# Kernel tuning notes

Hardware: AMD Instinct MI355X
Metric: run time of the kernel (lower is better)

## Reference

```python
import jax, jax.numpy as jnp
import numpy as np

L, B, T, C, H, V, CTX = 4, 2, 1024, 1024, 16, 50257, 2048
D = C // H
EPS = 1e-5
NEG_SLOPE = 0.01


def layer_norm(x, w, b):
    mu = jnp.mean(x, axis=-1, keepdims=True)
    var = jnp.mean(jnp.square(x - mu), axis=-1, keepdims=True)
    return (x - mu) * jax.lax.rsqrt(var + EPS) * w + b


def setup_inputs() -> dict:
    key = jax.random.key(0)
    ks = jax.random.split(key, 8)
    s = 0.02  # init std as in _init_weights
    return {
        "idx": jax.random.randint(ks[0], (B, T), 0, V),
        "wte": jax.random.normal(ks[1], (V, C), jnp.float32) * s,
        "wpe": jax.random.normal(ks[2], (CTX, C), jnp.float32) * s,
        "ln1_w": jnp.ones((L, C), jnp.float32),
        "ln1_b": jnp.zeros((L, C), jnp.float32),
        "attn_w": jax.random.normal(ks[3], (L, C, 3 * C), jnp.float32) * s,
        "attn_b": jnp.zeros((L, 3 * C), jnp.float32),
        "proj_w": jax.random.normal(ks[4], (L, C, C), jnp.float32) * s,
        "proj_b": jnp.zeros((L, C), jnp.float32),
        "ln2_w": jnp.ones((L, C), jnp.float32),
        "ln2_b": jnp.zeros((L, C), jnp.float32),
        "fc_w": jax.random.normal(ks[5], (L, C, 4 * C), jnp.float32) * s,
        "fc_b": jnp.zeros((L, 4 * C), jnp.float32),
        "fcproj_w": jax.random.normal(ks[6], (L, 4 * C, C), jnp.float32) * s,
        "fcproj_b": jnp.zeros((L, C), jnp.float32),
        "lnf_w": jnp.ones((C,), jnp.float32),
        "lnf_b": jnp.zeros((C,), jnp.float32),
    }


def reference(idx, wte, wpe, ln1_w, ln1_b, attn_w, attn_b, proj_w, proj_b,
              ln2_w, ln2_b, fc_w, fc_b, fcproj_w, fcproj_b, lnf_w, lnf_b):
    t = idx.shape[1]
    x = wte[idx] + wpe[:t]  # [B,T,C]; dropout=0 => identity
    causal = jnp.tril(jnp.ones((t, t), bool))  # [T,T]
    scale = 1.0 / np.sqrt(D)
    for l in range(L):
        # --- causal self-attention ---
        h = layer_norm(x, ln1_w[l], ln1_b[l])
        qkv = h @ attn_w[l] + attn_b[l]  # [B,T,3C]
        q, k, v = jnp.split(qkv, 3, axis=-1)
        q = q.reshape(B, t, H, D)
        k = k.reshape(B, t, H, D)
        v = v.reshape(B, t, H, D)
        att = jnp.einsum('bthd,bshd->bhts', q, k) * scale  # [B,H,T,T]
        att = jnp.where(causal, att, -jnp.inf)
        att = jax.nn.softmax(att, axis=-1)
        y = jnp.einsum('bhts,bshd->bthd', att, v).reshape(B, t, C)
        x = x + y @ proj_w[l] + proj_b[l]
        # --- MLP ---
        h = layer_norm(x, ln2_w[l], ln2_b[l])
        h = h @ fc_w[l] + fc_b[l]
        h = jnp.where(h >= 0, h, NEG_SLOPE * h)  # LeakyReLU(0.01)
        x = x + h @ fcproj_w[l] + fcproj_b[l]
    x = layer_norm(x, lnf_w, lnf_b)
    # targets=None path: lm_head on last position only, tied weight = wte
    logits = x[:, -1:, :] @ wte.T  # [B,1,V]
    return logits
```

## Files before the change

### kernel.cpp

```cpp
#include <hip/hip_runtime.h>
#include <hip/hip_bf16.h>


#define TT 1024
#define CC 1024
#define NHEAD 16
#define DHEAD 64
#define NBATCH 2
#define VOCAB 50257

typedef __attribute__((ext_vector_type(8))) short bf16x8;
typedef __attribute__((ext_vector_type(4))) float f32x4;

#define GPTR(p) (const __attribute__((address_space(1))) void*)(p)
#define LPTR(p) (__attribute__((address_space(3))) void*)(p)

__device__ __forceinline__ unsigned short f2bf(float f) {
  union { float f; unsigned u; } v; v.f = f;
  unsigned r = v.u + 0x7fffu + ((v.u >> 16) & 1u);
  return (unsigned short)(r >> 16);
}
__device__ __forceinline__ float bf2f(unsigned short u) {
  union { unsigned u; float f; } v; v.u = ((unsigned)u) << 16;
  return v.f;
}

__device__ __forceinline__ f32x4 mfma_bf16(bf16x8 a, bf16x8 b, f32x4 c) {
  return __builtin_amdgcn_mfma_f32_16x16x32_bf16(a, b, c, 0, 0, 0);
}

__device__ __forceinline__ unsigned pk2(float lo, float hi) {
  return (unsigned)f2bf(lo) | ((unsigned)f2bf(hi) << 16);
}

__global__ __launch_bounds__(256) void embedln_k(const int* __restrict__ idx,
    const float* __restrict__ wte, const float* __restrict__ wpe,
    const float* __restrict__ lw, const float* __restrict__ lb,
    float* __restrict__ x, unsigned short* __restrict__ h)
{
  __shared__ float rs[4], rss[4];
  const int row = blockIdx.x;
  const int t = row & (TT - 1);
  const int tok = idx[row];
  const int tid = threadIdx.x, wave = tid >> 6, lane = tid & 63;
  float4 va = ((const float4*)(wte + (size_t)tok * CC))[tid];
  float4 vp = ((const float4*)(wpe + (size_t)t * CC))[tid];
  float4 v = make_float4(va.x + vp.x, va.y + vp.y, va.z + vp.z, va.w + vp.w);
  ((float4*)(x + (size_t)row * CC))[tid] = v;
  float s  = v.x + v.y + v.z + v.w;
  float ss = v.x*v.x + v.y*v.y + v.z*v.z + v.w*v.w;
#pragma unroll
  for (int off = 1; off < 64; off <<= 1) {
    s  += __shfl_xor(s, off, 64);
    ss += __shfl_xor(ss, off, 64);
  }
  if (lane == 0) { rs[wave] = s; rss[wave] = ss; }
  __syncthreads();
  s  = rs[0] + rs[1] + rs[2] + rs[3];
  ss = rss[0] + rss[1] + rss[2] + rss[3];
  float mu = s * (1.f / CC);
  float var = ss * (1.f / CC) - mu * mu;
  float rstd = rsqrtf(var + 1e-5f);
  float4 wv = ((const float4*)lw)[tid];
  float4 bv = ((const float4*)lb)[tid];
  float o0 = (v.x - mu) * rstd * wv.x + bv.x;
  float o1 = (v.y - mu) * rstd * wv.y + bv.y;
  float o2 = (v.z - mu) * rstd * wv.z + bv.z;
  float o3 = (v.w - mu) * rstd * wv.w + bv.w;
  ((uint2*)(h + (size_t)row * CC))[tid] = make_uint2(pk2(o0, o1), pk2(o2, o3));
}

__global__ __launch_bounds__(256) void redln_k(float* __restrict__ x,
    const unsigned short* __restrict__ P, const float* __restrict__ bias,
    const float* __restrict__ lw, const float* __restrict__ lb,
    unsigned short* __restrict__ out, int splits)
{
  int row = blockIdx.x * 4 + (threadIdx.x >> 6);
  int lane = threadIdx.x & 63;
  const int c0 = lane * 16;
  float* xw = x + (size_t)row * CC + c0;
  float4 v[4];
#pragma unroll
  for (int i = 0; i < 4; ++i) v[i] = *(const float4*)(xw + i * 4);
  {
    const float4* b4 = (const float4*)(bias + c0);
#pragma unroll
    for (int i = 0; i < 4; ++i) {
      float4 bv = b4[i];
      v[i].x += bv.x; v[i].y += bv.y; v[i].z += bv.z; v[i].w += bv.w;
    }
  }
  for (int sp = 0; sp < splits; ++sp) {
    const unsigned short* pp = P + ((size_t)sp * 2048 + row) * CC + c0;
    bf16x8 pa = *(const bf16x8*)pp;
    bf16x8 pb = *(const bf16x8*)(pp + 8);
    v[0].x += bf2f((unsigned short)pa[0]); v[0].y += bf2f((unsigned short)pa[1]);
    v[0].z += bf2f((unsigned short)pa[2]); v[0].w += bf2f((unsigned short)pa[3]);
    v[1].x += bf2f((unsigned short)pa[4]); v[1].y += bf2f((unsigned short)pa[5]);
    v[1].z += bf2f((unsigned short)pa[6]); v[1].w += bf2f((unsigned short)pa[7]);
    v[2].x += bf2f((unsigned short)pb[0]); v[2].y += bf2f((unsigned short)pb[1]);
    v[2].z += bf2f((unsigned short)pb[2]); v[2].w += bf2f((unsigned short)pb[3]);
    v[3].x += bf2f((unsigned short)pb[4]); v[3].y += bf2f((unsigned short)pb[5]);
    v[3].z += bf2f((unsigned short)pb[6]); v[3].w += bf2f((unsigned short)pb[7]);
  }
  float s = 0.f, ss = 0.f;
#pragma unroll
  for (int i = 0; i < 4; ++i) {
    *(float4*)(xw + i * 4) = v[i];
    s  += v[i].x + v[i].y + v[i].z + v[i].w;
    ss += v[i].x*v[i].x + v[i].y*v[i].y + v[i].z*v[i].z + v[i].w*v[i].w;
  }
#pragma unroll
  for (int off = 1; off < 64; off <<= 1) {
    s  += __shfl_xor(s, off, 64);
    ss += __shfl_xor(ss, off, 64);
  }
  float mu = s * (1.f / CC);
  float var = ss * (1.f / CC) - mu * mu;
  float rstd = rsqrtf(var + 1e-5f);
  const float* wr = lw + c0;
  const float* br = lb + c0;
  unsigned q[8];
#pragma unroll
  for (int i = 0; i < 4; ++i) {
    float4 wv = *(const float4*)(wr + i * 4);
    float4 bv = *(const float4*)(br + i * 4);
    float o0 = (v[i].x - mu) * rstd * wv.x + bv.x;
    float o1 = (v[i].y - mu) * rstd * wv.y + bv.y;
    float o2 = (v[i].z - mu) * rstd * wv.z + bv.z;
    float o3 = (v[i].w - mu) * rstd * wv.w + bv.w;
    q[i*2+0] = pk2(o0, o1);
    q[i*2+1] = pk2(o2, o3);
  }
  uint4* op = (uint4*)(out + (size_t)row * CC + c0);
  op[0] = make_uint4(q[0], q[1], q[2], q[3]);
  op[1] = make_uint4(q[4], q[5], q[6], q[7]);
}

__global__ __launch_bounds__(256) void wconv_all_k(
    const float* __restrict__ attn_w, unsigned short* __restrict__ wt_attn,
    const float* __restrict__ proj_w, unsigned short* __restrict__ wt_proj,
    const float* __restrict__ fc_w,   unsigned short* __restrict__ wt_fc,
    const float* __restrict__ fcp_w,  unsigned short* __restrict__ wt_fcp)
{
  int b = blockIdx.x;
  const float* W; unsigned short* Wt; int K, N, kx, ny;
  if (b < 3072) {
    int layer = b / 768, tI = b % 768;
    K = 1024; N = 3072;
    W = attn_w + (size_t)layer * K * N; Wt = wt_attn + (size_t)layer * K * N;
    kx = tI % 16; ny = tI / 16;
  } else if (b < 3840) {
    b -= 3072; int layer = b / 256, tI = b % 256;
    K = 1024; N = 1024;
    W = proj_w + (size_t)layer * K * N; Wt = wt_proj + (size_t)layer * K * N;
    kx = tI % 16; ny = tI / 16;
  } else if (b < 6912) {
    b -= 3840; int layer = b / 1024, tI = b % 1024;
    K = 1024; N = 4096;
    W = fc_w + (size_t)layer * K * N; Wt = wt_fc + (size_t)layer * K * N;
    kx = tI % 16; ny = tI / 16;
  } else {
    b -= 6912; int layer = b / 1024, tI = b % 1024;
    K = 4096; N = 1024;
    W = fcp_w + (size_t)layer * K * N; Wt = wt_fcp + (size_t)layer * K * N;
    kx = tI % 64; ny = tI / 64;
  }
  __shared__ float tile[64][65];
  const int k0 = kx << 6, n0 = ny << 6;
  const int t = threadIdx.x;
  {
    const int r = t >> 4, c4 = t & 15;
#pragma unroll
    for (int p = 0; p < 4; ++p) {
      int kr = r + (p << 4);
      float4 v = *(const float4*)(W + (size_t)(k0 + kr) * N + n0 + (c4 << 2));
      tile[kr][(c4 << 2) + 0] = v.x;
      tile[kr][(c4 << 2) + 1] = v.y;
      tile[kr][(c4 << 2) + 2] = v.z;
      tile[kr][(c4 << 2) + 3] = v.w;
    }
  }
  __syncthreads();
  {
    const int n = t >> 2, kq = t & 3;
    bf16x8 o0, o1;
#pragma unroll
    for (int e = 0; e < 8; ++e) o0[e] = (short)f2bf(tile[(kq << 4) + e][n]);
#pragma unroll
    for (int e = 0; e < 8; ++e) o1[e] = (short)f2bf(tile[(kq << 4) + 8 + e][n]);
    unsigned short* dst = Wt + (size_t)(n0 + n) * K + k0 + (kq << 4);
    *(bf16x8*)dst = o0;
    *(bf16x8*)(dst + 8) = o1;
  }
}

#define MODE_QKV  0
#define MODE_PART 1
#define MODE_FC   2

template<int MODE>
__global__ __launch_bounds__(256) void gemm_k(
    const unsigned short* __restrict__ A,
    const unsigned short* __restrict__ Wt,
    const float* __restrict__ bias,
    unsigned short* __restrict__ obf,
    unsigned short* __restrict__ q_o,
    unsigned short* __restrict__ k_o,
    unsigned short* __restrict__ v_o,
    int M, int N, int K, int kchunk, int ncol0)
{
  __shared__ alignas(16) unsigned short Asm[2][128 * 64];
  __shared__ alignas(16) unsigned short Bsm[2][128 * 64];
  const int tid  = threadIdx.x;
  const int wave = tid >> 6, lane = tid & 63;
  const int lg = lane >> 4, ll = lane & 15;
  const int nTM = M >> 7, nTN = N >> 7;
  int bid = blockIdx.x;
  const int mt = bid % nTM; bid /= nTM;
  const int nt = bid % nTN;
  const int s  = bid / nTN;
  const int m0 = mt << 7, n0 = nt << 7;
  const int kb = s * kchunk;
  const int nIter = kchunk >> 6;
  const int wm = (wave >> 1) << 6, wn = (wave & 1) << 6;
  f32x4 acc[4][4] = {};

#define STAGE(BUF, K0)                                                        \
  {                                                                           \
    _Pragma("unroll")                                                         \
    for (int c = 0; c < 4; ++c) {                                             \
      const int seg = (wave << 2) + c;                                        \
      const int g = (seg << 6) + lane;                                        \
      const int row = g >> 3, kq = g & 7;                                     \
      const unsigned short* asrc = A  + (size_t)(m0 + row) * K + (K0) + (kq << 3); \
      const unsigned short* bsrc = Wt + (size_t)(n0 + row) * K + (K0) + (kq << 3); \
      __builtin_amdgcn_global_load_lds(GPTR(asrc), LPTR(&Asm[BUF][seg << 9]), 16, 0, 0); \
      __builtin_amdgcn_global_load_lds(GPTR(bsrc), LPTR(&Bsm[BUF][seg << 9]), 16, 0, 0); \
    }                                                                         \
  }

  STAGE(0, kb);
  if (nIter > 1) STAGE(1, kb + 64);

  for (int t = 0; t < nIter; ++t) {
    const int cur = t & 1;
    if (t + 1 < nIter) { asm volatile("s_waitcnt vmcnt(8)" ::: "memory"); }
    else               { asm volatile("s_waitcnt vmcnt(0)" ::: "memory"); }
    __builtin_amdgcn_sched_barrier(0);
    __builtin_amdgcn_s_barrier();

    const unsigned short* As = &Asm[cur][0];
    const unsigned short* Bs = &Bsm[cur][0];
#pragma unroll
    for (int kk = 0; kk < 2; ++kk) {
      bf16x8 af[4], bfr[4];
#pragma unroll
      for (int i = 0; i < 4; ++i)
        af[i] = *(const bf16x8*)(As + ((wm + i * 16 + ll) << 6) + (kk << 5) + (lg << 3));
#pragma unroll
      for (int j = 0; j < 4; ++j)
        bfr[j] = *(const bf16x8*)(Bs + ((wn + j * 16 + ll) << 6) + (kk << 5) + (lg << 3));
#pragma unroll
      for (int i = 0; i < 4; ++i)
#pragma unroll
        for (int j = 0; j < 4; ++j)
          acc[i][j] = mfma_bf16(af[i], bfr[j], acc[i][j]);
    }
    __builtin_amdgcn_sched_barrier(0);
    __builtin_amdgcn_s_barrier();
    if (t + 2 < nIter) STAGE(cur, kb + ((t + 2) << 6));
  }
#undef STAGE

#pragma unroll
  for (int j = 0; j < 4; ++j) {
    int gc = n0 + wn + j * 16 + ll;
    int gcol = ncol0 + gc;
    float bv = (MODE == MODE_PART) ? 0.f : bias[gcol];
#pragma unroll
    for (int i = 0; i < 4; ++i) {
      int gr0 = m0 + wm + i * 16 + (lg << 2);
#pragma unroll
      for (int r = 0; r < 4; ++r) {
        int grow = gr0 + r;
        float val = acc[i][j][r] + bv;
        if (MODE == MODE_QKV) {
          int which = gcol >> 10;
          int head = (gcol >> 6) & 15;
          int d = gcol & 63;
          int bb = grow >> 10, tt2 = grow & (TT - 1);
          size_t bhb = ((size_t)((bb << 4) + head)) << 16;
          if (which == 2)      v_o[bhb + ((size_t)d << 10) + tt2] = f2bf(val);
          else if (which == 1) k_o[bhb + ((size_t)tt2 << 6) + d] = f2bf(val);
          else                 q_o[bhb + ((size_t)tt2 << 6) + d] = f2bf(val);
        } else if (MODE == MODE_FC) {
          val = (val >= 0.f) ? val : 0.01f * val;
          obf[(size_t)grow * N + gc] = f2bf(val);
        } else {
          obf[((size_t)s * M + grow) * N + gc] = f2bf(val);
        }
      }
    }
  }
}

__global__ __launch_bounds__(256) void attn_k(
    const unsigned short* __restrict__ Qb,
    const unsigned short* __restrict__ Kb,
    const unsigned short* __restrict__ Vb,
    unsigned short* __restrict__ ybuf)
{
  __shared__ alignas(16) unsigned short Ksm[64][72];
  __shared__ alignas(16) unsigned short Vtsm[64][64];
  __shared__ alignas(16) unsigned short Psm[4][16][72];
  const int tid = threadIdx.x;
  const int wave = tid >> 6, lane = tid & 63;
  const int lg = lane >> 4, ll = lane & 15;
  const int qt = blockIdx.x & 15, bh = blockIdx.x >> 4;
  const int b = bh >> 4, h = bh & 15;
  const size_t base = (size_t)bh << 16;
  const int q0 = qt << 6;
  const float SC = 0.125f * 1.44269504f;

  const int qrow = q0 + wave * 16 + ll;
  bf16x8 aq0 = *(const bf16x8*)(Qb + base + ((size_t)qrow << 6) + (lg << 3));
  bf16x8 aq1 = *(const bf16x8*)(Qb + base + ((size_t)qrow << 6) + 32 + (lg << 3));

  f32x4 accy[4] = {};
  float m_run[4], l_run[4];
#pragma unroll
  for (int r = 0; r < 4; ++r) { m_run[r] = -1e30f; l_run[r] = 0.f; }

  const int sk_row = tid >> 3, sk_cq = tid & 7;
  const int sv_d = tid & 63, sv_kq = tid >> 6;
  const int qg0 = q0 + wave * 16 + (lg << 2);

  for (int kb = 0; kb <= qt; ++kb) {
    const int kbase = kb << 6;
#pragma unroll
    for (int p = 0; p < 2; ++p) {
      int r = sk_row + (p << 5);
      bf16x8 kv = *(const bf16x8*)(Kb + base + ((size_t)(kbase + r) << 6) + (sk_cq << 3));
      *(bf16x8*)&Ksm[r][sk_cq << 3] = kv;
    }
#pragma unroll
    for (int p = 0; p < 2; ++p) {
      int kq8 = sv_kq + (p << 2);
      bf16x8 wv = *(const bf16x8*)(Vb + base + ((size_t)sv_d << 10) + kbase + (kq8 << 3));
      int u = kq8 ^ (sv_d & 7);
      *(bf16x8*)&Vtsm[sv_d][u << 3] = wv;
    }
    __syncthreads();

    float p_[4][4];
    float rmax[4] = {-1e30f, -1e30f, -1e30f, -1e30f};
#pragma unroll
    for (int kk = 0; kk < 4; ++kk) {
      f32x4 z = {};
      bf16x8 bk0 = *(const bf16x8*)&Ksm[kk * 16 + ll][lg << 3];
      bf16x8 bk1 = *(const bf16x8*)&Ksm[kk * 16 + ll][32 + (lg << 3)];
      z = mfma_bf16(aq0, bk0, z);
      z = mfma_bf16(aq1, bk1, z);
      int key = kbase + kk * 16 + ll;
#pragma unroll
      for (int r = 0; r < 4; ++r) {
        float v = z[r] * SC;
        v = (key > qg0 + r) ? -1e30f : v;
        p_[kk][r] = v;
        rmax[r] = fmaxf(rmax[r], v);
      }
    }
#pragma unroll
    for (int off = 1; off < 16; off <<= 1)
#pragma unroll
      for (int r = 0; r < 4; ++r)
        rmax[r] = fmaxf(rmax[r], __shfl_xor(rmax[r], off, 64));

    float alpha[4], rsum[4];
#pragma unroll
    for (int r = 0; r < 4; ++r) {
      float mn = fmaxf(m_run[r], rmax[r]);
      alpha[r] = exp2f(m_run[r] - mn);
      m_run[r] = mn;
      rsum[r] = 0.f;
    }
#pragma unroll
    for (int kk = 0; kk < 4; ++kk)
#pragma unroll
      for (int r = 0; r < 4; ++r) {
        float e = exp2f(p_[kk][r] - m_run[r]);
        p_[kk][r] = e;
        rsum[r] += e;
      }
#pragma unroll
    for (int off = 1; off < 16; off <<= 1)
#pragma unroll
      for (int r = 0; r < 4; ++r)
        rsum[r] += __shfl_xor(rsum[r], off, 64);
#pragma unroll
    for (int r = 0; r < 4; ++r)
      l_run[r] = l_run[r] * alpha[r] + rsum[r];
#pragma unroll
    for (int df = 0; df < 4; ++df)
#pragma unroll
      for (int r = 0; r < 4; ++r)
        accy[df][r] *= alpha[r];

#pragma unroll
    for (int kk = 0; kk < 4; ++kk)
#pragma unroll
      for (int r = 0; r < 4; ++r)
        Psm[wave][(lg << 2) + r][kk * 16 + ll] = f2bf(p_[kk][r]);
    bf16x8 pa0 = *(const bf16x8*)&Psm[wave][ll][lg << 3];
    bf16x8 pa1 = *(const bf16x8*)&Psm[wave][ll][32 + (lg << 3)];

#pragma unroll
    for (int df = 0; df < 4; ++df) {
      int d = df * 16 + ll;
      int u0 = lg ^ (d & 7);
      int u1 = (4 + lg) ^ (d & 7);
      bf16x8 bv0 = *(const bf16x8*)&Vtsm[d][u0 << 3];
      bf16x8 bv1 = *(const bf16x8*)&Vtsm[d][u1 << 3];
      accy[df] = mfma_bf16(pa0, bv0, accy[df]);
      accy[df] = mfma_bf16(pa1, bv1, accy[df]);
    }
    __syncthreads();
  }

#pragma unroll
  for (int df = 0; df < 4; ++df)
#pragma unroll
    for (int r = 0; r < 4; ++r) {
      int qr = qg0 + r;
      float y = accy[df][r] / l_run[r];
      ybuf[(((size_t)((b << 10) + qr)) << 10) + (h << 6) + df * 16 + ll] = f2bf(y);
    }
}


__global__ __launch_bounds__(256) void qlast_k(
    const unsigned short* __restrict__ hbuf,
    const float* __restrict__ Wq,
    float* __restrict__ qpart)
{
  __shared__ float xs[2][128];
  const int tid = threadIdx.x, ks = blockIdx.y;
  {
    const int b = tid >> 7, j = tid & 127;
    xs[b][j] = bf2f(hbuf[((size_t)(b * TT + TT - 1)) * CC + ks * 128 + j]);
  }
  __syncthreads();
  const int n = blockIdx.x * 256 + tid;
  float a0 = 0.f, a1 = 0.f;
  const float* wp = Wq + (size_t)(ks * 128) * 3072 + n;
  for (int k = 0; k < 128; k += 8)
#pragma unroll
    for (int u = 0; u < 8; ++u) {
      float w = wp[(size_t)(k + u) * 3072];
      a0 += xs[0][k + u] * w;
      a1 += xs[1][k + u] * w;
    }
  qpart[(size_t)(ks * 2 + 0) * 1024 + n] = a0;
  qpart[(size_t)(ks * 2 + 1) * 1024 + n] = a1;
}

__global__ __launch_bounds__(256) void attnlast2_k(
    const float* __restrict__ qpart, const float* __restrict__ bq,
    const unsigned short* __restrict__ Kb,
    const unsigned short* __restrict__ Vb,
    float* __restrict__ y_last)
{
  __shared__ float qs[64];
  __shared__ float wm[4], wl[4], wacc[4][64];
  const int tid = threadIdx.x;
  const int wave = tid >> 6, lane = tid & 63;
  const int bh = blockIdx.x;
  const int b = bh >> 4, h = bh & 15;
  const size_t base = (size_t)bh << 16;
  if (tid < 64) {
    const int col = h * 64 + tid;
    float q = bq[col];
#pragma unroll
    for (int ks = 0; ks < 8; ++ks)
      q += qpart[(size_t)(ks * 2 + b) * 1024 + col];
    qs[tid] = q;
  }
  __syncthreads();

  float m_w = -1e30f, l_w = 0.f, acc = 0.f;
  for (int ks = 0; ks < 4; ++ks) {
    const int key = ks * 256 + wave * 64 + lane;
    float s = 0.f;
    const unsigned short* kp = Kb + base + ((size_t)key << 6);
#pragma unroll
    for (int o = 0; o < 8; ++o) {
      bf16x8 kv = *(const bf16x8*)(kp + (o << 3));
#pragma unroll
      for (int e = 0; e < 8; ++e)
        s += qs[(o << 3) + e] * bf2f((unsigned short)kv[e]);
    }
    s *= 0.125f;
    float m = s;
#pragma unroll
    for (int off = 1; off < 64; off <<= 1)
      m = fmaxf(m, __shfl_xor(m, off, 64));
    float mn = fmaxf(m_w, m);
    float alpha = __expf(m_w - mn);
    m_w = mn;
    float p = __expf(s - mn);
    float ps = p;
#pragma unroll
    for (int off = 1; off < 64; off <<= 1)
      ps += __shfl_xor(ps, off, 64);
    l_w = l_w * alpha + ps;
    float a2 = 0.f;
    const unsigned short* vp = Vb + base + ((size_t)lane << 10) + ks * 256 + wave * 64;
#pragma unroll
    for (int j8 = 0; j8 < 8; ++j8) {
      bf16x8 vv = *(const bf16x8*)(vp + (j8 << 3));
#pragma unroll
      for (int e = 0; e < 8; ++e) {
        float pj = __shfl(p, (j8 << 3) + e, 64);
        a2 += pj * bf2f((unsigned short)vv[e]);
      }
    }
    acc = acc * alpha + a2;
  }
  if (lane == 0) { wm[wave] = m_w; wl[wave] = l_w; }
  wacc[wave][lane] = acc;
  __syncthreads();
  if (wave == 0) {
    float m0 = fmaxf(fmaxf(wm[0], wm[1]), fmaxf(wm[2], wm[3]));
    float lt = 0.f, at = 0.f;
#pragma unroll
    for (int sI = 0; sI < 4; ++sI) {
      float f = __expf(wm[sI] - m0);
      lt += wl[sI] * f;
      at += wacc[sI][lane] * f;
    }
    y_last[b * CC + h * 64 + lane] = at / lt;
  }
}

__global__ __launch_bounds__(256) void projpart_k(
    const float* __restrict__ ylast,
    const float* __restrict__ W,
    float* __restrict__ ppart)
{
  __shared__ float xs[2][128];
  const int tid = threadIdx.x, ks = blockIdx.y;
  {
    const int b = tid >> 7, j = tid & 127;
    xs[b][j] = ylast[b * 1024 + ks * 128 + j];
  }
  __syncthreads();
  const int n = blockIdx.x * 256 + tid;
  float a0 = 0.f, a1 = 0.f;
  const float* wp = W + (size_t)(ks * 128) * 1024 + n;
  for (int k = 0; k < 128; k += 8)
#pragma unroll
    for (int u = 0; u < 8; ++u) {
      float w = wp[(size_t)(k + u) * 1024];
      a0 += xs[0][k + u] * w;
      a1 += xs[1][k + u] * w;
    }
  ppart[(size_t)(ks * 2 + 0) * 1024 + n] = a0;
  ppart[(size_t)(ks * 2 + 1) * 1024 + n] = a1;
}

__global__ __launch_bounds__(256) void fclast_k(
    const float* __restrict__ x, const float* __restrict__ ppart,
    const float* __restrict__ pbias,
    const float* __restrict__ lw, const float* __restrict__ lb,
    const float* __restrict__ W,
    float* __restrict__ fcpart)
{
  __shared__ float xs[2][1024];
  const int tid = threadIdx.x;
  const int wave = tid >> 6, lane = tid & 63;
  if (wave < 2) {
    const int c0 = lane * 16;
    const float* xr = x + ((size_t)(wave * TT + TT - 1)) * CC + c0;
    float4 v[4];
    float s = 0.f, ss = 0.f;
#pragma unroll
    for (int i = 0; i < 4; ++i) {
      v[i] = *(const float4*)(xr + i * 4);
      float4 bv = *(const float4*)(pbias + c0 + i * 4);
      v[i].x += bv.x; v[i].y += bv.y; v[i].z += bv.z; v[i].w += bv.w;
    }
#pragma unroll
    for (int sp = 0; sp < 8; ++sp) {
      const float* pp = ppart + (size_t)(sp * 2 + wave) * 1024 + c0;
#pragma unroll
      for (int i = 0; i < 4; ++i) {
        float4 pv = *(const float4*)(pp + i * 4);
        v[i].x += pv.x; v[i].y += pv.y; v[i].z += pv.z; v[i].w += pv.w;
      }
    }
#pragma unroll
    for (int i = 0; i < 4; ++i) {
      s  += v[i].x + v[i].y + v[i].z + v[i].w;
      ss += v[i].x*v[i].x + v[i].y*v[i].y + v[i].z*v[i].z + v[i].w*v[i].w;
    }
#pragma unroll
    for (int off = 1; off < 64; off <<= 1) {
      s  += __shfl_xor(s, off, 64);
      ss += __shfl_xor(ss, off, 64);
    }
    float mu = s * (1.f / CC);
    float var = ss * (1.f / CC) - mu * mu;
    float rstd = rsqrtf(var + 1e-5f);
#pragma unroll
    for (int i = 0; i < 4; ++i) {
      float4 wv = *(const float4*)(lw + c0 + i * 4);
      float4 bv = *(const float4*)(lb + c0 + i * 4);
      xs[wave][c0 + i * 4 + 0] = (v[i].x - mu) * rstd * wv.x + bv.x;
      xs[wave][c0 + i * 4 + 1] = (v[i].y - mu) * rstd * wv.y + bv.y;
      xs[wave][c0 + i * 4 + 2] = (v[i].z - mu) * rstd * wv.z + bv.z;
      xs[wave][c0 + i * 4 + 3] = (v[i].w - mu) * rstd * wv.w + bv.w;
    }
  }
  __syncthreads();
  const int ks = blockIdx.y;
  const int n = blockIdx.x * 256 + tid;
  float a0 = 0.f, a1 = 0.f;
  const float* wp = W + (size_t)(ks * 128) * 4096 + n;
  for (int k = 0; k < 128; k += 8)
#pragma unroll
    for (int u = 0; u < 8; ++u) {
      float w = wp[(size_t)(k + u) * 4096];
      a0 += xs[0][ks * 128 + k + u] * w;
      a1 += xs[1][ks * 128 + k + u] * w;
    }
  fcpart[(size_t)(ks * 2 + 0) * 4096 + n] = a0;
  fcpart[(size_t)(ks * 2 + 1) * 4096 + n] = a1;
}

__global__ __launch_bounds__(256) void fcprojpart_k(
    const float* __restrict__ fcpart, const float* __restrict__ fcbias,
    const float* __restrict__ W,
    float* __restrict__ fppart)
{
  __shared__ float hs[2][512];
  const int tid = threadIdx.x, ks = blockIdx.y;
#pragma unroll
  for (int i = 0; i < 4; ++i) {
    const int e = tid + 256 * i;
    const int b = e >> 9, j = e & 511;
    const int c = ks * 512 + j;
    float v = fcbias[c];
#pragma unroll
    for (int sp = 0; sp < 8; ++sp)
      v += fcpart[(size_t)(sp * 2 + b) * 4096 + c];
    hs[b][j] = (v >= 0.f) ? v : 0.01f * v;
  }
  __syncthreads();
  const int n = blockIdx.x * 256 + tid;
  float a0 = 0.f, a1 = 0.f;
  const float* wp = W + (size_t)(ks * 512) * 1024 + n;
  for (int k = 0; k < 512; k += 8)
#pragma unroll
    for (int u = 0; u < 8; ++u) {
      float w = wp[(size_t)(k + u) * 1024];
      a0 += hs[0][k + u] * w;
      a1 += hs[1][k + u] * w;
    }
  fppart[(size_t)(ks * 2 + 0) * 1024 + n] = a0;
  fppart[(size_t)(ks * 2 + 1) * 1024 + n] = a1;
}

__global__ __launch_bounds__(256) void lnfmerge_k(const float* __restrict__ x,
    const float* __restrict__ ppart, const float* __restrict__ pbias,
    const float* __restrict__ fppart, const float* __restrict__ fpbias,
    const float* __restrict__ lw, const float* __restrict__ lb,
    float* __restrict__ xf)
{
  __shared__ float rs[4], rss[4];
  const int row = blockIdx.x;
  const int tid = threadIdx.x;
  const int wave = tid >> 6, lane = tid & 63;
  const int c0 = tid * 4;
  float4 v = *(const float4*)(x + ((size_t)(row * TT + TT - 1)) * CC + c0);
  {
    float4 b1 = *(const float4*)(pbias + c0);
    float4 b2 = *(const float4*)(fpbias + c0);
    v.x += b1.x + b2.x; v.y += b1.y + b2.y;
    v.z += b1.z + b2.z; v.w += b1.w + b2.w;
  }
#pragma unroll
  for (int sp = 0; sp < 8; ++sp) {
    float4 a = *(const float4*)(ppart + (size_t)(sp * 2 + row) * 1024 + c0);
    float4 b = *(const float4*)(fppart + (size_t)(sp * 2 + row) * 1024 + c0);
    v.x += a.x + b.x; v.y += a.y + b.y;
    v.z += a.z + b.z; v.w += a.w + b.w;
  }
  float s  = v.x + v.y + v.z + v.w;
  float ss = v.x*v.x + v.y*v.y + v.z*v.z + v.w*v.w;
#pragma unroll
  for (int off = 1; off < 64; off <<= 1) {
    s  += __shfl_xor(s, off, 64);
    ss += __shfl_xor(ss, off, 64);
  }
  if (lane == 0) { rs[wave] = s; rss[wave] = ss; }
  __syncthreads();
  s  = rs[0] + rs[1] + rs[2] + rs[3];
  ss = rss[0] + rss[1] + rss[2] + rss[3];
  float mu = s * (1.f / CC);
  float var = ss * (1.f / CC) - mu * mu;
  float rstd = rsqrtf(var + 1e-5f);
  float4 wv = *(const float4*)(lw + c0);
  float4 bv = *(const float4*)(lb + c0);
  float4 o;
  o.x = (v.x - mu) * rstd * wv.x + bv.x;
  o.y = (v.y - mu) * rstd * wv.y + bv.y;
  o.z = (v.z - mu) * rstd * wv.z + bv.z;
  o.w = (v.w - mu) * rstd * wv.w + bv.w;
  *(float4*)(xf + (size_t)row * CC + c0) = o;
}

__global__ __launch_bounds__(256) void head_k(const float* __restrict__ xf,
    const float* __restrict__ wte, float* __restrict__ out)
{
  int v = (blockIdx.x << 2) + (threadIdx.x >> 6);
  if (v >= VOCAB) return;
  int lane = threadIdx.x & 63;
  const float4* wr = (const float4*)(wte + (size_t)v * CC);
  const float4* x0 = (const float4*)xf;
  const float4* x1 = (const float4*)(xf + CC);
  float a0 = 0.f, a1 = 0.f;
#pragma unroll
  for (int i = 0; i < 4; ++i) {
    float4 wv = wr[lane + i * 64];
    float4 p0 = x0[lane + i * 64];
    float4 p1 = x1[lane + i * 64];
    a0 += wv.x * p0.x + wv.y * p0.y + wv.z * p0.z + wv.w * p0.w;
    a1 += wv.x * p1.x + wv.y * p1.y + wv.z * p1.z + wv.w * p1.w;
  }
#pragma unroll
  for (int off = 1; off < 64; off <<= 1) {
    a0 += __shfl_xor(a0, off, 64);
    a1 += __shfl_xor(a1, off, 64);
  }
  if (lane == 0) {
    out[v] = a0;
    out[VOCAB + v] = a1;
  }
}

extern "C" void kernel_launch(void* const* d_in, const int* in_sizes, int n_in,
                              void* d_out, int out_size, void* d_ws, size_t ws_size,
                              hipStream_t stream)
{
  const int*   idx      = (const int*)d_in[0];
  const float* wte      = (const float*)d_in[1];
  const float* wpe      = (const float*)d_in[2];
  const float* ln1_w    = (const float*)d_in[3];
  const float* ln1_b    = (const float*)d_in[4];
  const float* attn_w   = (const float*)d_in[5];
  const float* attn_b   = (const float*)d_in[6];
  const float* proj_w   = (const float*)d_in[7];
  const float* proj_b   = (const float*)d_in[8];
  const float* ln2_w    = (const float*)d_in[9];
  const float* ln2_b    = (const float*)d_in[10];
  const float* fc_w     = (const float*)d_in[11];
  const float* fc_b     = (const float*)d_in[12];
  const float* fcproj_w = (const float*)d_in[13];
  const float* fcproj_b = (const float*)d_in[14];
  const float* lnf_w    = (const float*)d_in[15];
  const float* lnf_b    = (const float*)d_in[16];
  float* out = (float*)d_out;

  const size_t MB = 1u << 20;
  char* ws = (char*)d_ws;
  float*          x   = (float*)ws;
  unsigned short* h   = (unsigned short*)(ws + 8*MB);
  unsigned short* qb  = (unsigned short*)(ws + 12*MB);
  unsigned short* kb_ = (unsigned short*)(ws + 16*MB);
  unsigned short* vb  = (unsigned short*)(ws + 20*MB);
  unsigned short* yb  = (unsigned short*)(ws + 24*MB);
  unsigned short* hf  = (unsigned short*)(ws + 28*MB);
  char* sm = ws + 44*MB;
  float* xf     = (float*)(sm + 0);
  float* ylast  = (float*)(sm + 16*1024);
  float* qpart  = (float*)(sm + 64*1024);
  float* ppart  = (float*)(sm + 128*1024);
  float* fppart = (float*)(sm + 192*1024);
  float* fcpart = (float*)(sm + 256*1024);
  unsigned short* wt_attn   = (unsigned short*)(ws + 46*MB);
  unsigned short* wt_proj   = (unsigned short*)(ws + 70*MB);
  unsigned short* wt_fc     = (unsigned short*)(ws + 76*MB);
  unsigned short* wt_fcproj = (unsigned short*)(ws + 100*MB);
  unsigned short* Ppart     = (unsigned short*)(ws + 124*MB);

  embedln_k<<<NBATCH * TT, 256, 0, stream>>>(idx, wte, wpe, ln1_w, ln1_b, x, h);

  wconv_all_k<<<9984, 256, 0, stream>>>(attn_w, wt_attn, proj_w, wt_proj,
                                        fc_w, wt_fc, fcproj_w, wt_fcproj);

  for (int l = 0; l < 3; ++l) {
    gemm_k<MODE_QKV><<<16 * 24, 256, 0, stream>>>(h,
        wt_attn + (size_t)l * 3072 * 1024, attn_b + (size_t)l * 3 * CC,
        nullptr, qb, kb_, vb, 2048, 3072, 1024, 1024, 0);
    attn_k<<<NBATCH * NHEAD * 16, 256, 0, stream>>>(qb, kb_, vb, yb);
    gemm_k<MODE_PART><<<16 * 8 * 4, 256, 0, stream>>>(yb,
        wt_proj + (size_t)l * 1024 * 1024, nullptr,
        Ppart, nullptr, nullptr, nullptr, 2048, 1024, 1024, 256, 0);
    redln_k<<<512, 256, 0, stream>>>(x, Ppart, proj_b + l * CC,
        ln2_w + l * CC, ln2_b + l * CC, h, 4);
    gemm_k<MODE_FC><<<16 * 32, 256, 0, stream>>>(h,
        wt_fc + (size_t)l * 1024 * 4096, fc_b + (size_t)l * 4 * CC,
        hf, nullptr, nullptr, nullptr, 2048, 4096, 1024, 1024, 0);
    gemm_k<MODE_PART><<<16 * 8 * 4, 256, 0, stream>>>(hf,
        wt_fcproj + (size_t)l * 4096 * 1024, nullptr,
        Ppart, nullptr, nullptr, nullptr, 2048, 1024, 4096, 1024, 0);
    redln_k<<<512, 256, 0, stream>>>(x, Ppart, fcproj_b + l * CC,
        ln1_w + (l + 1) * CC, ln1_b + (l + 1) * CC, h, 4);
  }

  {
    const int l = 3;
    gemm_k<MODE_QKV><<<16 * 16, 256, 0, stream>>>(h,
        wt_attn + (size_t)l * 3072 * 1024 + (size_t)1024 * 1024,
        attn_b + (size_t)l * 3 * CC,
        nullptr, qb, kb_, vb, 2048, 2048, 1024, 1024, 1024);
    qlast_k<<<dim3(4, 8), 256, 0, stream>>>(h,
        attn_w + (size_t)l * CC * 3 * CC, qpart);
    attnlast2_k<<<32, 256, 0, stream>>>(qpart, attn_b + (size_t)l * 3 * CC,
        kb_, vb, ylast);
    projpart_k<<<dim3(4, 8), 256, 0, stream>>>(ylast,
        proj_w + (size_t)l * CC * CC, ppart);
    fclast_k<<<dim3(16, 8), 256, 0, stream>>>(x, ppart, proj_b + l * CC,
        ln2_w + l * CC, ln2_b + l * CC,
        fc_w + (size_t)l * CC * 4 * CC, fcpart);
    fcprojpart_k<<<dim3(4, 8), 256, 0, stream>>>(fcpart,
        fc_b + (size_t)l * 4 * CC, fcproj_w + (size_t)l * 4 * CC * CC, fppart);
    lnfmerge_k<<<2, 256, 0, stream>>>(x, ppart, proj_b + l * CC,
        fppart, fcproj_b + l * CC, lnf_w, lnf_b, xf);
  }

  head_k<<<(VOCAB + 3) / 4, 256, 0, stream>>>(xf, wte, out);
}
```

Baseline: 668.1 us.

## Switch GEMM to 32x32x16 MFMA with XOR-swizzled LDS layout

The tiled GEMM now uses 32x32x16 bf16 MFMA instructions with a 2x2 accumulator grid per wave instead of 16x16x32 with 4x4. The global-to-LDS staging XOR-swizzles the 16-byte k chunks by row, and the fragment reads apply the same swizzle to avoid LDS bank conflicts. The goal is fewer LDS reads and MFMA issues per k-step plus conflict-free shared memory access. The epilogue row/column mapping changes to match the 32x32 output layout, so a mapping mistake would break correctness.

```diff
diff --git a/kernel.cpp b/kernel.cpp
--- a/kernel.cpp
+++ b/kernel.cpp
@@ -11,6 +11,7 @@
 
 typedef __attribute__((ext_vector_type(8))) short bf16x8;
 typedef __attribute__((ext_vector_type(4))) float f32x4;
+typedef __attribute__((ext_vector_type(16))) float f32x16;
 
 #define GPTR(p) (const __attribute__((address_space(1))) void*)(p)
 #define LPTR(p) (__attribute__((address_space(3))) void*)(p)
@@ -27,6 +28,9 @@
 
 __device__ __forceinline__ f32x4 mfma_bf16(bf16x8 a, bf16x8 b, f32x4 c) {
   return __builtin_amdgcn_mfma_f32_16x16x32_bf16(a, b, c, 0, 0, 0);
+}
+__device__ __forceinline__ f32x16 mfma32_bf16(bf16x8 a, bf16x8 b, f32x16 c) {
+  return __builtin_amdgcn_mfma_f32_32x32x16_bf16(a, b, c, 0, 0, 0);
 }
 
 __device__ __forceinline__ unsigned pk2(float lo, float hi) {
@@ -214,7 +218,7 @@
   __shared__ alignas(16) unsigned short Bsm[2][128 * 64];
   const int tid  = threadIdx.x;
   const int wave = tid >> 6, lane = tid & 63;
-  const int lg = lane >> 4, ll = lane & 15;
+  const int rl = lane & 31, hi = lane >> 5;
   const int nTM = M >> 7, nTN = N >> 7;
   int bid = blockIdx.x;
   const int mt = bid % nTM; bid /= nTM;
@@ -224,7 +228,7 @@
   const int kb = s * kchunk;
   const int nIter = kchunk >> 6;
   const int wm = (wave >> 1) << 6, wn = (wave & 1) << 6;
-  f32x4 acc[4][4] = {};
+  f32x16 acc[2][2] = {};
 
 #define STAGE(BUF, K0)                                                        \
   {                                                                           \
@@ -233,8 +237,9 @@
       const int seg = (wave << 2) + c;                                        \
       const int g = (seg << 6) + lane;                                        \
       const int row = g >> 3, kq = g & 7;                                     \
-      const unsigned short* asrc = A  + (size_t)(m0 + row) * K + (K0) + (kq << 3); \
-      const unsigned short* bsrc = Wt + (size_t)(n0 + row) * K + (K0) + (kq << 3); \
+      const int kqs = kq ^ (row & 7);                                         \
+      const unsigned short* asrc = A  + (size_t)(m0 + row) * K + (K0) + (kqs << 3); \
+      const unsigned short* bsrc = Wt + (size_t)(n0 + row) * K + (K0) + (kqs << 3); \
       __builtin_amdgcn_global_load_lds(GPTR(asrc), LPTR(&Asm[BUF][seg << 9]), 16, 0, 0); \
       __builtin_amdgcn_global_load_lds(GPTR(bsrc), LPTR(&Bsm[BUF][seg << 9]), 16, 0, 0); \
     }                                                                         \
@@ -253,19 +258,17 @@
     const unsigned short* As = &Asm[cur][0];
     const unsigned short* Bs = &Bsm[cur][0];
 #pragma unroll
-    for (int kk = 0; kk < 2; ++kk) {
-      bf16x8 af[4], bfr[4];
-#pragma unroll
-      for (int i = 0; i < 4; ++i)
-        af[i] = *(const bf16x8*)(As + ((wm + i * 16 + ll) << 6) + (kk << 5) + (lg << 3));
-#pragma unroll
-      for (int j = 0; j < 4; ++j)
-        bfr[j] = *(const bf16x8*)(Bs + ((wn + j * 16 + ll) << 6) + (kk << 5) + (lg << 3));
-#pragma unroll
-      for (int i = 0; i < 4; ++i)
-#pragma unroll
-        for (int j = 0; j < 4; ++j)
-          acc[i][j] = mfma_bf16(af[i], bfr[j], acc[i][j]);
+    for (int sl = 0; sl < 4; ++sl) {
+      const int c = sl * 2 + hi;
+      const int cs = (c ^ (rl & 7)) << 3;
+      bf16x8 a0 = *(const bf16x8*)(As + ((wm + rl) << 6) + cs);
+      bf16x8 a1 = *(const bf16x8*)(As + ((wm + 32 + rl) << 6) + cs);
+      bf16x8 b0 = *(const bf16x8*)(Bs + ((wn + rl) << 6) + cs);
+      bf16x8 b1 = *(const bf16x8*)(Bs + ((wn + 32 + rl) << 6) + cs);
+      acc[0][0] = mfma32_bf16(a0, b0, acc[0][0]);
+      acc[0][1] = mfma32_bf16(a0, b1, acc[0][1]);
+      acc[1][0] = mfma32_bf16(a1, b0, acc[1][0]);
+      acc[1][1] = mfma32_bf16(a1, b1, acc[1][1]);
     }
     __builtin_amdgcn_sched_barrier(0);
     __builtin_amdgcn_s_barrier();
@@ -274,17 +277,17 @@
 #undef STAGE
 
 #pragma unroll
-  for (int j = 0; j < 4; ++j) {
-    int gc = n0 + wn + j * 16 + ll;
+  for (int j = 0; j < 2; ++j) {
+    int gc = n0 + wn + j * 32 + rl;
     int gcol = ncol0 + gc;
     float bv = (MODE == MODE_PART) ? 0.f : bias[gcol];
 #pragma unroll
-    for (int i = 0; i < 4; ++i) {
-      int gr0 = m0 + wm + i * 16 + (lg << 2);
-#pragma unroll
-      for (int r = 0; r < 4; ++r) {
-        int grow = gr0 + r;
-        float val = acc[i][j][r] + bv;
+    for (int i = 0; i < 2; ++i) {
+      int gr0 = m0 + wm + i * 32 + 4 * hi;
+#pragma unroll
+      for (int reg = 0; reg < 16; ++reg) {
+        int grow = gr0 + (reg & 3) + 8 * (reg >> 2);
+        float val = acc[i][j][reg] + bv;
         if (MODE == MODE_QKV) {
           int which = gcol >> 10;
           int head = (gcol >> 6) & 15;
```

Result: faster. 648.7 us (-2.9%).
